# Kernel tuning notes

Measured on AMD Instinct MI355X. Metric: run time of the kernel, lower is better.

Reference implementation:

```python
import jax, jax.numpy as jnp
import numpy as np

SIM_THRESHOLD = 0.65  # recall() returns decoded memory only if best_sim > 0.65
EPS = 1e-8            # torch F.cosine_similarity default eps


def setup_inputs() -> dict:
    key = jax.random.key(0)
    k1, k2, k3, k4 = jax.random.split(key, 4)
    dim, seq, n_mem = 1024, 2048, 131072
    bound = 1.0 / np.sqrt(dim)  # nn.Linear default init scale
    return {
        "query": jax.random.normal(k1, (seq, dim), dtype=jnp.float32),
        "bank": jax.random.normal(k2, (n_mem, dim), dtype=jnp.float32),
        "w_dec": jax.random.uniform(k3, (dim, dim), dtype=jnp.float32, minval=-bound, maxval=bound),
        "b_dec": jax.random.uniform(k4, (dim,), dtype=jnp.float32, minval=-bound, maxval=bound),
    }


def reference(query, bank, w_dec, b_dec):
    # q = query.detach().mean(dim=0)
    q = query.mean(axis=0)                                   # [dim]
    # cosine similarity of q against every stored memory (batched version of
    # the per-item F.cosine_similarity loop): dot / (max(||a||,eps)*max(||b||,eps))
    q_norm = jnp.maximum(jnp.linalg.norm(q), EPS)
    bank_norms = jnp.maximum(jnp.linalg.norm(bank, axis=1), EPS)  # [N]
    sims = (bank @ q) / (bank_norms * q_norm)                 # [N]
    idx = jnp.argmax(sims)
    best_sim = sims[idx]
    best_mem = bank[idx]                                      # [dim]
    # decoder(best.embedding): Linear(dim, dim)
    decoded = best_mem @ w_dec.T + b_dec                      # [dim]
    # original returns None below threshold; model as zeros to keep static shape
    return jnp.where(best_sim > SIM_THRESHOLD, decoded, jnp.zeros_like(decoded))
```

## Files before the change

### kernel.cpp

```cpp
#include <hip/hip_runtime.h>

#define EPS 1e-8f
#define THR 0.65f

constexpr int DIM  = 1024;
constexpr int SEQ  = 2048;
constexpr int NMEM = 131072;

constexpr int SIM_BLKS = 2048;
constexpr int ROWS_PER_WAVE = NMEM / (SIM_BLKS * 4);

typedef float f4 __attribute__((ext_vector_type(4)));

constexpr int WS_Q     = 262144;
constexpr int WS_SSP   = 263168;
constexpr int WS_BESTS = 263178;

__global__ void qsumA_kernel(const float* __restrict__ query, float* __restrict__ ws) {
    int t = threadIdx.x;
    int b = blockIdx.x;
    const f4* qp = (const f4*)(query + (size_t)b * 8 * DIM) + t;
    f4 s = qp[0];
    #pragma unroll
    for (int r = 1; r < 8; ++r) s += qp[r * 256];
    ((f4*)ws)[b * 256 + t] = s;
}

__global__ void qsumB_kernel(float* __restrict__ ws) {
    __shared__ f4 lds[256];
    int t = threadIdx.x;
    int j = blockIdx.x;
    int fc    = 32 * j + (t & 31);
    int chunk = t >> 5;
    const f4* pf = (const f4*)ws;
    f4 s = pf[(32 * chunk) * 256 + fc];
    #pragma unroll
    for (int i = 1; i < 32; ++i) s += pf[(32 * chunk + i) * 256 + fc];
    lds[t] = s;
    __syncthreads();
    if (t < 32) {
        f4 f = lds[t];
        #pragma unroll
        for (int c = 1; c < 8; ++c) f += lds[t + 32 * c];
        f *= (1.0f / (float)SEQ);
        ((f4*)(ws + WS_Q))[32 * j + t] = f;
        float ss = f.x * f.x + f.y * f.y + f.z * f.z + f.w * f.w;
        #pragma unroll
        for (int m = 16; m >= 1; m >>= 1) ss += __shfl_xor(ss, m);
        if (t == 0) ws[WS_SSP + j] = ss;
    }
}

__device__ __forceinline__ unsigned int float_to_ordered(float f) {
    unsigned int b = __float_as_uint(f);
    return (b & 0x80000000u) ? ~b : (b | 0x80000000u);
}

__device__ __forceinline__ unsigned long long pack_best(float sim, int idx) {
    return ((unsigned long long)float_to_ordered(sim) << 32) |
           (unsigned int)(~(unsigned int)idx);
}

__launch_bounds__(256)
__global__ void sim_kernel(const float* __restrict__ bank, const float* __restrict__ ws,
                           unsigned long long* __restrict__ bests) {
    __shared__ unsigned long long wbest[4];
    int tid  = threadIdx.x;
    int lane = tid & 63;
    int wid  = tid >> 6;

    float ssq = ws[WS_SSP + 0];
    #pragma unroll
    for (int j = 1; j < 8; ++j) ssq += ws[WS_SSP + j];
    float qn = fmaxf(sqrtf(ssq), EPS);

    const f4* q4 = (const f4*)(ws + WS_Q);
    f4 q0 = q4[lane +   0];
    f4 q1 = q4[lane +  64];
    f4 q2 = q4[lane + 128];
    f4 q3 = q4[lane + 192];

    int gw   = blockIdx.x * 4 + wid;
    int row0 = gw * ROWS_PER_WAVE;

    float bestSim = -1e30f;
    int   bestIdx = 0;

    #pragma unroll
    for (int g = 0; g < ROWS_PER_WAVE / 4; ++g) {
        float dot[4], ss[4];
        f4 b[4][4];
        #pragma unroll
        for (int r = 0; r < 4; ++r) {
            const f4* bp = (const f4*)(bank + (size_t)(row0 + g * 4 + r) * DIM);
            b[r][0] = __builtin_nontemporal_load(bp + lane +   0);
            b[r][1] = __builtin_nontemporal_load(bp + lane +  64);
            b[r][2] = __builtin_nontemporal_load(bp + lane + 128);
            b[r][3] = __builtin_nontemporal_load(bp + lane + 192);
        }
        #pragma unroll
        for (int r = 0; r < 4; ++r) {
            dot[r] = b[r][0].x*q0.x + b[r][0].y*q0.y + b[r][0].z*q0.z + b[r][0].w*q0.w
                   + b[r][1].x*q1.x + b[r][1].y*q1.y + b[r][1].z*q1.z + b[r][1].w*q1.w
                   + b[r][2].x*q2.x + b[r][2].y*q2.y + b[r][2].z*q2.z + b[r][2].w*q2.w
                   + b[r][3].x*q3.x + b[r][3].y*q3.y + b[r][3].z*q3.z + b[r][3].w*q3.w;
            ss[r]  = b[r][0].x*b[r][0].x + b[r][0].y*b[r][0].y + b[r][0].z*b[r][0].z + b[r][0].w*b[r][0].w
                   + b[r][1].x*b[r][1].x + b[r][1].y*b[r][1].y + b[r][1].z*b[r][1].z + b[r][1].w*b[r][1].w
                   + b[r][2].x*b[r][2].x + b[r][2].y*b[r][2].y + b[r][2].z*b[r][2].z + b[r][2].w*b[r][2].w
                   + b[r][3].x*b[r][3].x + b[r][3].y*b[r][3].y + b[r][3].z*b[r][3].z + b[r][3].w*b[r][3].w;
        }
        #pragma unroll
        for (int m = 32; m >= 1; m >>= 1) {
            #pragma unroll
            for (int r = 0; r < 4; ++r) {
                dot[r] += __shfl_xor(dot[r], m);
                ss[r]  += __shfl_xor(ss[r], m);
            }
        }
        #pragma unroll
        for (int r = 0; r < 4; ++r) {
            float bn  = fmaxf(sqrtf(ss[r]), EPS);
            float sim = dot[r] / (bn * qn);
            if (sim > bestSim) { bestSim = sim; bestIdx = row0 + g * 4 + r; }
        }
    }

    if (lane == 0) wbest[wid] = pack_best(bestSim, bestIdx);
    __syncthreads();
    if (tid == 0) {
        unsigned long long p = wbest[0];
        if (wbest[1] > p) p = wbest[1];
        if (wbest[2] > p) p = wbest[2];
        if (wbest[3] > p) p = wbest[3];
        bests[blockIdx.x] = p;
    }
}

__global__ void decode_kernel(const float* __restrict__ bank,
                              const float* __restrict__ w_dec,
                              const float* __restrict__ b_dec,
                              const unsigned long long* __restrict__ bests,
                              float* __restrict__ out) {
    __shared__ unsigned long long red[256];
    __shared__ float mem[DIM];
    int tid = threadIdx.x;

    unsigned long long p = bests[tid];
    #pragma unroll
    for (int i = 1; i < SIM_BLKS / 256; ++i) {
        unsigned long long v = bests[tid + i * 256];
        if (v > p) p = v;
    }
    red[tid] = p;
    __syncthreads();
    #pragma unroll
    for (int s = 128; s >= 1; s >>= 1) {
        if (tid < s) {
            if (red[tid + s] > red[tid]) red[tid] = red[tid + s];
        }
        __syncthreads();
    }
    p = red[0];
    unsigned int u = (unsigned int)(p >> 32);
    unsigned int fb = (u & 0x80000000u) ? (u & 0x7FFFFFFFu) : ~u;
    float sim = __uint_as_float(fb);
    int idx   = (int)(~(unsigned int)(p & 0xFFFFFFFFu));

    ((float4*)mem)[tid] = ((const float4*)(bank + (size_t)idx * DIM))[tid];
    __syncthreads();

    bool ok  = sim > THR;
    int lane = tid & 63, wid = tid >> 6;
    int row  = blockIdx.x * 4 + wid;

    const float4* wp = (const float4*)(w_dec + (size_t)row * DIM);
    const float4* m4 = (const float4*)mem;
    float dot = 0.f;
    #pragma unroll
    for (int it = 0; it < 4; ++it) {
        float4 w = wp[lane + it * 64];
        float4 m = m4[lane + it * 64];
        dot += w.x * m.x + w.y * m.y + w.z * m.z + w.w * m.w;
    }
    #pragma unroll
    for (int m = 32; m >= 1; m >>= 1) dot += __shfl_xor(dot, m);

    if (lane == 0) out[row] = ok ? (dot + b_dec[row]) : 0.0f;
}

extern "C" void kernel_launch(void* const* d_in, const int* in_sizes, int n_in,
                              void* d_out, int out_size, void* d_ws, size_t ws_size,
                              hipStream_t stream) {
    const float* query = (const float*)d_in[0];
    const float* bank  = (const float*)d_in[1];
    const float* w_dec = (const float*)d_in[2];
    const float* b_dec = (const float*)d_in[3];
    float* out = (float*)d_out;
    float* ws  = (float*)d_ws;
    unsigned long long* bests = (unsigned long long*)(ws + WS_BESTS);

    qsumA_kernel<<<256, 256, 0, stream>>>(query, ws);
    qsumB_kernel<<<8, 256, 0, stream>>>(ws);
    sim_kernel<<<SIM_BLKS, 256, 0, stream>>>(bank, ws, bests);
    decode_kernel<<<256, 256, 0, stream>>>(bank, w_dec, b_dec, bests, out);
}
```

Before: 106.3 us.

## Fuse query mean into single last-block reduction kernel, drop nontemporal loads

Merges the two query-sum kernels into one launch of 64 blocks, where the last block to finish (tracked by an atomic counter) reduces the partials and writes the mean vector and its clamped norm. The sim kernel now reads a precomputed norm, bank loads switch from nontemporal to ordinary loads, and the decode kernel's argmax reduction uses wave shuffles instead of an LDS tree. This removes one launch and some redundant per-block work, at the cost of fewer blocks for the query sum. The counter is never reset; the modulo test keeps it correct across repeated calls only if the workspace starts at a multiple of 64.

Result: slower. 124.7 us (+17.3%).

```diff
diff --git a/kernel.cpp b/kernel.cpp
--- a/kernel.cpp
+++ b/kernel.cpp
@@ -7,48 +7,49 @@
 constexpr int SEQ  = 2048;
 constexpr int NMEM = 131072;
 
+constexpr int QBLKS    = 64;
 constexpr int SIM_BLKS = 2048;
 constexpr int ROWS_PER_WAVE = NMEM / (SIM_BLKS * 4);
 
 typedef float f4 __attribute__((ext_vector_type(4)));
 
-constexpr int WS_Q     = 262144;
-constexpr int WS_SSP   = 263168;
-constexpr int WS_BESTS = 263178;
-
-__global__ void qsumA_kernel(const float* __restrict__ query, float* __restrict__ ws) {
+constexpr int WS_PART  = 0;
+constexpr int WS_Q     = 65536;
+constexpr int WS_QN    = 66560;
+constexpr int WS_BESTS = 66562;
+constexpr int WS_CNT   = 70658;
+
+__global__ void qsum_kernel(const float* __restrict__ query, float* __restrict__ ws) {
     int t = threadIdx.x;
     int b = blockIdx.x;
-    const f4* qp = (const f4*)(query + (size_t)b * 8 * DIM) + t;
+    const f4* qp = (const f4*)(query + (size_t)b * 32 * DIM) + t;
     f4 s = qp[0];
     #pragma unroll
-    for (int r = 1; r < 8; ++r) s += qp[r * 256];
-    ((f4*)ws)[b * 256 + t] = s;
-}
-
-__global__ void qsumB_kernel(float* __restrict__ ws) {
-    __shared__ f4 lds[256];
-    int t = threadIdx.x;
-    int j = blockIdx.x;
-    int fc    = 32 * j + (t & 31);
-    int chunk = t >> 5;
-    const f4* pf = (const f4*)ws;
-    f4 s = pf[(32 * chunk) * 256 + fc];
-    #pragma unroll
-    for (int i = 1; i < 32; ++i) s += pf[(32 * chunk + i) * 256 + fc];
-    lds[t] = s;
-    __syncthreads();
-    if (t < 32) {
-        f4 f = lds[t];
-        #pragma unroll
-        for (int c = 1; c < 8; ++c) f += lds[t + 32 * c];
-        f *= (1.0f / (float)SEQ);
-        ((f4*)(ws + WS_Q))[32 * j + t] = f;
-        float ss = f.x * f.x + f.y * f.y + f.z * f.z + f.w * f.w;
-        #pragma unroll
-        for (int m = 16; m >= 1; m >>= 1) ss += __shfl_xor(ss, m);
-        if (t == 0) ws[WS_SSP + j] = ss;
-    }
+    for (int r = 1; r < 32; ++r) s += qp[r * 256];
+    ((f4*)(ws + WS_PART))[b * 256 + t] = s;
+
+    __threadfence();
+    __shared__ unsigned done_old;
+    if (t == 0) done_old = atomicAdd((unsigned*)(ws + WS_CNT), 1u);
+    __syncthreads();
+    if ((done_old & (QBLKS - 1)) != QBLKS - 1) return;
+    __threadfence();
+
+    const f4* pf = (const f4*)(ws + WS_PART);
+    f4 q = pf[t];
+    #pragma unroll
+    for (int b2 = 1; b2 < QBLKS; ++b2) q += pf[b2 * 256 + t];
+    q *= (1.0f / (float)SEQ);
+    ((f4*)(ws + WS_Q))[t] = q;
+
+    float ss = q.x * q.x + q.y * q.y + q.z * q.z + q.w * q.w;
+    #pragma unroll
+    for (int m = 32; m >= 1; m >>= 1) ss += __shfl_xor(ss, m);
+    __shared__ float red[4];
+    int lane = t & 63, wid = t >> 6;
+    if (lane == 0) red[wid] = ss;
+    __syncthreads();
+    if (t == 0) ws[WS_QN] = fmaxf(sqrtf(red[0] + red[1] + red[2] + red[3]), EPS);
 }
 
 __device__ __forceinline__ unsigned int float_to_ordered(float f) {
@@ -69,10 +70,7 @@
     int lane = tid & 63;
     int wid  = tid >> 6;
 
-    float ssq = ws[WS_SSP + 0];
-    #pragma unroll
-    for (int j = 1; j < 8; ++j) ssq += ws[WS_SSP + j];
-    float qn = fmaxf(sqrtf(ssq), EPS);
+    float qn = ws[WS_QN];
 
     const f4* q4 = (const f4*)(ws + WS_Q);
     f4 q0 = q4[lane +   0];
@@ -93,10 +91,10 @@
         #pragma unroll
         for (int r = 0; r < 4; ++r) {
             const f4* bp = (const f4*)(bank + (size_t)(row0 + g * 4 + r) * DIM);
-            b[r][0] = __builtin_nontemporal_load(bp + lane +   0);
-            b[r][1] = __builtin_nontemporal_load(bp + lane +  64);
-            b[r][2] = __builtin_nontemporal_load(bp + lane + 128);
-            b[r][3] = __builtin_nontemporal_load(bp + lane + 192);
+            b[r][0] = bp[lane +   0];
+            b[r][1] = bp[lane +  64];
+            b[r][2] = bp[lane + 128];
+            b[r][3] = bp[lane + 192];
         }
         #pragma unroll
         for (int r = 0; r < 4; ++r) {
@@ -141,9 +139,10 @@
                               const float* __restrict__ b_dec,
                               const unsigned long long* __restrict__ bests,
                               float* __restrict__ out) {
-    __shared__ unsigned long long red[256];
+    __shared__ unsigned long long wred[4];
     __shared__ float mem[DIM];
     int tid = threadIdx.x;
+    int lane = tid & 63, wid = tid >> 6;
 
     unsigned long long p = bests[tid];
     #pragma unroll
@@ -151,16 +150,18 @@
         unsigned long long v = bests[tid + i * 256];
         if (v > p) p = v;
     }
-    red[tid] = p;
-    __syncthreads();
-    #pragma unroll
-    for (int s = 128; s >= 1; s >>= 1) {
-        if (tid < s) {
-            if (red[tid + s] > red[tid]) red[tid] = red[tid + s];
-        }
-        __syncthreads();
-    }
-    p = red[0];
+    #pragma unroll
+    for (int m = 32; m >= 1; m >>= 1) {
+        unsigned long long v = __shfl_xor(p, m);
+        if (v > p) p = v;
+    }
+    if (lane == 0) wred[wid] = p;
+    __syncthreads();
+    p = wred[0];
+    if (wred[1] > p) p = wred[1];
+    if (wred[2] > p) p = wred[2];
+    if (wred[3] > p) p = wred[3];
+
     unsigned int u = (unsigned int)(p >> 32);
     unsigned int fb = (u & 0x80000000u) ? (u & 0x7FFFFFFFu) : ~u;
     float sim = __uint_as_float(fb);
@@ -169,9 +170,8 @@
     ((float4*)mem)[tid] = ((const float4*)(bank + (size_t)idx * DIM))[tid];
     __syncthreads();
 
-    bool ok  = sim > THR;
-    int lane = tid & 63, wid = tid >> 6;
-    int row  = blockIdx.x * 4 + wid;
+    bool ok = sim > THR;
+    int row = blockIdx.x * 4 + wid;
 
     const float4* wp = (const float4*)(w_dec + (size_t)row * DIM);
     const float4* m4 = (const float4*)mem;
@@ -199,8 +199,7 @@
     float* ws  = (float*)d_ws;
     unsigned long long* bests = (unsigned long long*)(ws + WS_BESTS);
 
-    qsumA_kernel<<<256, 256, 0, stream>>>(query, ws);
-    qsumB_kernel<<<8, 256, 0, stream>>>(ws);
+    qsum_kernel<<<QBLKS, 256, 0, stream>>>(query, ws);
     sim_kernel<<<SIM_BLKS, 256, 0, stream>>>(bank, ws, bests);
     decode_kernel<<<256, 256, 0, stream>>>(bank, w_dec, b_dec, bests, out);
 }
```
